# Performance work log

Hardware: AMD Instinct MI355X
Metric: run time of the kernel (lower is better)

## Reference

```python
import jax, jax.numpy as jnp
import numpy as np
from jax import lax

B, CIN, COUT, H, W = 8, 256, 256, 96, 96


def _conv_bn(x, w, g, b, act):
    # 3x3 conv, stride 1, SAME padding (NCHW / OIHW), then per-channel affine (folded BN)
    y = lax.conv_general_dilated(x, w, (1, 1), 'SAME',
                                 dimension_numbers=('NCHW', 'OIHW', 'NCHW'))
    y = y * g[None, :, None, None] + b[None, :, None, None]
    return jax.nn.relu(y) if act else y


def setup_inputs() -> dict:
    key = jax.random.key(0)
    ks = jax.random.split(key, 16)
    def wgt(k, cout, cin):
        return jax.random.normal(k, (cout, cin, 3, 3), jnp.float32) * (1.0 / np.sqrt(cin * 9))
    def gb(k, c):
        k1, k2 = jax.random.split(k)
        return (1.0 + 0.1 * jax.random.normal(k1, (c,), jnp.float32),
                0.1 * jax.random.normal(k2, (c,), jnp.float32))
    g_p1, b_p1 = gb(ks[1], COUT); g_p2, b_p2 = gb(ks[3], COUT)
    g_p, b_p = gb(ks[5], COUT); g_c1, b_c1 = gb(ks[7], COUT); g_c2, b_c2 = gb(ks[9], COUT)
    return {
        'x': jax.random.normal(ks[0], (B, CIN, H, W), jnp.float32),
        'w_p1': wgt(ks[10], COUT, CIN), 'g_p1': g_p1, 'b_p1': b_p1,
        'w_p2': wgt(ks[11], COUT, CIN), 'g_p2': g_p2, 'b_p2': b_p2,
        'w_p': wgt(ks[12], COUT, COUT), 'g_p': g_p, 'b_p': b_p,
        'w_c1': wgt(ks[13], COUT, CIN), 'g_c1': g_c1, 'b_c1': b_c1,
        'w_c2': wgt(ks[14], COUT, COUT), 'g_c2': g_c2, 'b_c2': b_c2,
    }


def reference(x, w_p1, g_p1, b_p1, w_p2, g_p2, b_p2, w_p, g_p, b_p,
              w_c1, g_c1, b_c1, w_c2, g_c2, b_c2):
    # branch 1: conv -> TopPool (cummax up, i.e. reverse along H) -> BottomPool (cummax down)
    p1 = _conv_bn(x, w_p1, g_p1, b_p1, act=True)
    pool1 = lax.cummax(p1, axis=2, reverse=True)   # TopPool
    pool1 = lax.cummax(pool1, axis=2)              # BottomPool
    # branch 2: conv -> LeftPool (reverse along W) -> RightPool
    p2 = _conv_bn(x, w_p2, g_p2, b_p2, act=True)
    pool2 = lax.cummax(p2, axis=3, reverse=True)   # LeftPool
    pool2 = lax.cummax(pool2, axis=3)              # RightPool
    p_conv = _conv_bn(pool1 + pool2, w_p, g_p, b_p, act=False)
    conv1 = _conv_bn(x, w_c1, g_c1, b_c1, act=False)
    relu = jax.nn.relu(p_conv + conv1)
    return _conv_bn(relu, w_c2, g_c2, b_c2, act=True)
```

## Files before the change

kernel.cpp:

```cpp
#include <hip/hip_runtime.h>


typedef _Float16 f16x8 __attribute__((ext_vector_type(8)));
typedef _Float16 f16x4v __attribute__((ext_vector_type(4)));
typedef float f32x4 __attribute__((ext_vector_type(4)));

#define HP 98
#define WP 98
#define KTOT 2304
#define WSET (256*KTOT)
#define XPAD_E ((size_t)8*HP*WP*256)
#define UVP_E  ((size_t)8*98*256)
#define UV2_E  ((size_t)3*8*96*256)
#define WUV_SET 196608

__device__ __forceinline__ int xcd_swz(int bid, int nwg)
{
  return (bid & 7) * (nwg >> 3) + (bid >> 3);
}

#define BUF_Q 24576
#define SMEM_Q 49152

struct CtxQ {
  unsigned goff[6];
  unsigned lds_stage;
  unsigned aoff;
  int wl, quad, wv;
  int b, h0, w0;
};

template<int SW>
__device__ __forceinline__ CtxQ make_ctxQ(int spatial, int ch)
{
  CtxQ c;
  c.b = spatial / 36;
  const int tt = spatial - c.b * 36;
  const int ht = tt / 6, wt = tt - ht * 6;
  c.h0 = ht * 16; c.w0 = wt * 16;
  const int tid = threadIdx.x, lane = tid & 63;
  c.wv = tid >> 6;
  c.quad = lane >> 4; c.wl = lane & 15;
  c.aoff = (unsigned)((ch * 8 + c.wv * 2) * 512 + c.wl * 32 + c.quad * 8);
  const unsigned base_hw = (unsigned)(c.b * HP + c.h0) * WP + c.w0;
#pragma unroll
  for (int t = 0; t < 6; ++t) {
    int s = (c.wv * 6 + t) * 16 + (lane >> 2);
    if (s > 323) s = 323;
    const int x = s / 18, y = s - x * 18;
    const int wh = SW ? y : x, ww = SW ? x : y;
    c.goff[t] = (base_hw + (unsigned)(wh * WP + ww)) * 256u + (lane & 3) * 8u;
  }
  c.lds_stage = (unsigned)(c.wv * 6) * 1024u + (unsigned)lane * 16u;
  return c;
}

__device__ __forceinline__ void stage_cbQ(const _Float16* __restrict__ src,
                                          char* sbuf, const CtxQ& c, int buf, int cb)
{
  char* l0 = sbuf + buf * BUF_Q + c.lds_stage;
#pragma unroll
  for (int t = 0; t < 6; ++t) {
    const _Float16* g = src + c.goff[t] + cb * 32;
    __builtin_amdgcn_global_load_lds(
        (const __attribute__((address_space(1))) void*)g,
        (__attribute__((address_space(3))) void*)(l0 + t * 1024), 16, 0, 0);
  }
}

template<int TR>
__device__ __forceinline__ void conv_accumQ(const _Float16* __restrict__ src,
                                            const _Float16* __restrict__ wkb,
                                            char* sbuf, const CtxQ& c, f32x4 acc[2][16])
{
  const _Float16* A0 = wkb + c.aoff;
  stage_cbQ(src, sbuf, c, 0, 0);
#pragma unroll 1
  for (int cb = 0; cb < 8; ++cb) {
    __syncthreads();
    if (cb < 7) stage_cbQ(src, sbuf, c, (cb + 1) & 1, cb + 1);
    const _Float16* B = (const _Float16*)(sbuf + (cb & 1) * BUF_Q);
    const _Float16* A = A0 + cb * (9 * 8192);
#pragma unroll
    for (int o = 0; o < 3; ++o) {
      f16x8 af[3][2];
#pragma unroll
      for (int p = 0; p < 3; ++p) {
        const int tap = (TR == 0) ? p * 3 + o : o * 3 + p;
#pragma unroll
        for (int i = 0; i < 2; ++i)
          af[p][i] = *(const f16x8*)(A + tap * 8192 + i * 512);
      }
#pragma unroll
      for (int jh = 0; jh < 2; ++jh) {
        f16x8 cache[10];
#pragma unroll
        for (int r = 0; r < 10; ++r)
          cache[r] = *(const f16x8*)(B + ((jh * 8 + r) * 18 + c.wl + o) * 32 + c.quad * 8);
#pragma unroll
        for (int p = 0; p < 3; ++p)
#pragma unroll
          for (int i = 0; i < 2; ++i)
#pragma unroll
            for (int j = 0; j < 8; ++j)
              acc[i][jh * 8 + j] = __builtin_amdgcn_mfma_f32_16x16x32_f16(
                  af[p][i], cache[j + p], acc[i][jh * 8 + j], 0, 0, 0);
      }
    }
  }
  __syncthreads();
}

#define BUF_W 7168
#define SMEM_W 14336

struct Ctx4 {
  unsigned goff[2];
  unsigned lds_stage;
  unsigned aoff;
  int nrow;
  int wl, quad, wv;
  int b, h0, w0;
};

__device__ __forceinline__ Ctx4 make_ctx4(int spatial)
{
  Ctx4 c;
  c.b = spatial / 144;
  const int tt = spatial - c.b * 144;
  const int ht = tt / 6,  wt = tt - ht * 6;  c.h0 = ht * 4;  c.w0 = wt * 16;
  const int tid = threadIdx.x, lane = tid & 63;
  c.wv = tid >> 6;
  c.quad = lane >> 4; c.wl = lane & 15;
  c.aoff = (unsigned)(c.wv * 4 * 512 + c.wl * 32 + c.quad * 8);
  const unsigned base_hw = (unsigned)(c.b * HP + c.h0) * WP + c.w0;
  const int r0 = c.wv * 2;
  c.nrow = (c.wv < 3) ? 2 : 1;
#pragma unroll
  for (int t = 0; t < 2; ++t) {
    int row = r0 + t; if (row > 6) row = 6;
    int pos = row * 16 + (lane >> 2);
    if (pos > 107) pos = 107;
    const int wh = pos / 18, ww = pos - wh * 18;
    c.goff[t] = (base_hw + (unsigned)(wh * WP + ww)) * 256u + (lane & 3) * 8u;
  }
  c.lds_stage = (unsigned)r0 * 1024u + (unsigned)lane * 16u;
  return c;
}

__device__ __forceinline__ void stage_cb4(const _Float16* __restrict__ src,
                                          char* sbuf, const Ctx4& c, int buf, int cb)
{
  char* l0 = sbuf + buf * BUF_W + c.lds_stage;
#pragma unroll
  for (int t = 0; t < 2; ++t) {
    if (t < c.nrow) {
      const _Float16* g = src + c.goff[t] + cb * 32;
      __builtin_amdgcn_global_load_lds(
          (const __attribute__((address_space(1))) void*)g,
          (__attribute__((address_space(3))) void*)(l0 + t * 1024), 16, 0, 0);
    }
  }
}

__device__ __forceinline__ void conv_accum4(const _Float16* __restrict__ src,
                                            const _Float16* __restrict__ wkb,
                                            char* sbuf, const Ctx4& c, f32x4 acc[4][4])
{
  const _Float16* A0 = wkb + c.aoff;
  stage_cb4(src, sbuf, c, 0, 0);
#pragma unroll 1
  for (int cb = 0; cb < 8; ++cb) {
    __syncthreads();
    if (cb < 7) stage_cb4(src, sbuf, c, (cb + 1) & 1, cb + 1);
    const _Float16* B = (const _Float16*)(sbuf + (cb & 1) * BUF_W);
    const _Float16* A = A0 + cb * (9 * 8192);
#pragma unroll
    for (int o = 0; o < 3; ++o) {
      f16x8 cache[6];
#pragma unroll
      for (int r = 0; r < 6; ++r)
        cache[r] = *(const f16x8*)(B + (r * 18 + c.wl + o) * 32 + c.quad * 8);
#pragma unroll
      for (int p = 0; p < 3; ++p) {
        const int tap = p * 3 + o;
        f16x8 af[4];
#pragma unroll
        for (int i = 0; i < 4; ++i)
          af[i] = *(const f16x8*)(A + tap * 8192 + i * 512);
#pragma unroll
        for (int i = 0; i < 4; ++i)
#pragma unroll
          for (int j = 0; j < 4; ++j)
            acc[i][j] = __builtin_amdgcn_mfma_f32_16x16x32_f16(af[i], cache[j + p], acc[i][j], 0, 0, 0);
      }
    }
  }
  __syncthreads();
}

__global__ __launch_bounds__(256, 2) void k_conv_p12(
    const _Float16* __restrict__ xpad, const _Float16* __restrict__ wk,
    const float* __restrict__ bias1, const float* __restrict__ bias2,
    float* __restrict__ u_pad, float* __restrict__ v_pad)
{
  __shared__ __align__(16) char smem[SMEM_Q];
  const int lin = xcd_swz(blockIdx.x, 1152);
  const int set = lin >= 576;
  const int rem = lin - set * 576;
  const int spatial = rem >> 1, ch = rem & 1;
  f32x4 acc[2][16];
#pragma unroll
  for (int i = 0; i < 2; ++i)
#pragma unroll
    for (int j = 0; j < 16; ++j) acc[i][j] = (f32x4){0.f, 0.f, 0.f, 0.f};
  if (set == 0) {
    CtxQ c = make_ctxQ<0>(spatial, ch);
    conv_accumQ<0>(xpad, wk, smem, c, acc);
#pragma unroll
    for (int i = 0; i < 2; ++i) {
      const int co = (ch * 8 + c.wv * 2 + i) * 16 + c.quad * 4;
      const float4 bs = *(const float4*)(bias1 + co);
      float m0 = 0.f, m1 = 0.f, m2 = 0.f, m3 = 0.f;
#pragma unroll
      for (int j = 0; j < 16; ++j) {
        m0 = fmaxf(m0, acc[i][j][0] + bs.x);
        m1 = fmaxf(m1, acc[i][j][1] + bs.y);
        m2 = fmaxf(m2, acc[i][j][2] + bs.z);
        m3 = fmaxf(m3, acc[i][j][3] + bs.w);
      }
      unsigned* tgt = (unsigned*)(u_pad + ((size_t)c.b * 98 + (c.w0 + c.wl + 1)) * 256 + co);
      atomicMax(tgt + 0, __float_as_uint(m0));
      atomicMax(tgt + 1, __float_as_uint(m1));
      atomicMax(tgt + 2, __float_as_uint(m2));
      atomicMax(tgt + 3, __float_as_uint(m3));
    }
  } else {
    CtxQ c = make_ctxQ<1>(spatial, ch);
    conv_accumQ<1>(xpad, wk + WSET, smem, c, acc);
#pragma unroll
    for (int i = 0; i < 2; ++i) {
      const int co = (ch * 8 + c.wv * 2 + i) * 16 + c.quad * 4;
      const float4 bs = *(const float4*)(bias2 + co);
      float m0 = 0.f, m1 = 0.f, m2 = 0.f, m3 = 0.f;
#pragma unroll
      for (int j = 0; j < 16; ++j) {
        m0 = fmaxf(m0, acc[i][j][0] + bs.x);
        m1 = fmaxf(m1, acc[i][j][1] + bs.y);
        m2 = fmaxf(m2, acc[i][j][2] + bs.z);
        m3 = fmaxf(m3, acc[i][j][3] + bs.w);
      }
      unsigned* tgt = (unsigned*)(v_pad + ((size_t)c.b * 98 + (c.h0 + c.wl + 1)) * 256 + co);
      atomicMax(tgt + 0, __float_as_uint(m0));
      atomicMax(tgt + 1, __float_as_uint(m1));
      atomicMax(tgt + 2, __float_as_uint(m2));
      atomicMax(tgt + 3, __float_as_uint(m3));
    }
  }
}

__global__ __launch_bounds__(256, 2) void k_uv1d(
    const float* __restrict__ u_pad, const float* __restrict__ v_pad,
    const _Float16* __restrict__ wuv, float* __restrict__ u2, float* __restrict__ v2)
{
  const int id = blockIdx.x;
  const int b = id & 7, cs = (id >> 3) % 3, t = id / 24;
  const float* src = t ? v_pad : u_pad;
  float* dst = t ? v2 : u2;
  const _Float16* A0 = wuv + (size_t)(t * 3 + cs) * WUV_SET;
  const int lane = threadIdx.x & 63, wv = threadIdx.x >> 6;
  const int quad = lane >> 4, l16 = lane & 15;

  f32x4 acc[4][6];
#pragma unroll
  for (int i = 0; i < 4; ++i)
#pragma unroll
    for (int j = 0; j < 6; ++j) acc[i][j] = (f32x4){0.f, 0.f, 0.f, 0.f};

#pragma unroll 1
  for (int kb = 0; kb < 24; ++kb) {
    const int dw = kb >> 3, cb = kb & 7;
    f16x8 bf[6];
#pragma unroll
    for (int j = 0; j < 6; ++j) {
      const int pos = j * 16 + l16;
      const float* p = src + ((size_t)b * 98 + (pos + dw)) * 256 + cb * 32 + quad * 8;
      const float4 x0 = *(const float4*)p;
      const float4 x1 = *(const float4*)(p + 4);
      f16x8 v;
      v[0] = (_Float16)x0.x; v[1] = (_Float16)x0.y; v[2] = (_Float16)x0.z; v[3] = (_Float16)x0.w;
      v[4] = (_Float16)x1.x; v[5] = (_Float16)x1.y; v[6] = (_Float16)x1.z; v[7] = (_Float16)x1.w;
      bf[j] = v;
    }
    f16x8 af[4];
#pragma unroll
    for (int i = 0; i < 4; ++i)
      af[i] = *(const f16x8*)(A0 + (size_t)(kb * 16 + wv * 4 + i) * 512 + l16 * 32 + quad * 8);
#pragma unroll
    for (int i = 0; i < 4; ++i)
#pragma unroll
      for (int j = 0; j < 6; ++j)
        acc[i][j] = __builtin_amdgcn_mfma_f32_16x16x32_f16(af[i], bf[j], acc[i][j], 0, 0, 0);
  }
#pragma unroll
  for (int i = 0; i < 4; ++i)
#pragma unroll
    for (int j = 0; j < 6; ++j) {
      const int pos = j * 16 + l16;
      const int co = wv * 64 + i * 16 + quad * 4;
      *(f32x4*)(dst + ((size_t)(cs * 8 + b) * 96 + pos) * 256 + co) = acc[i][j];
    }
}

__global__ __launch_bounds__(256, 3) void k_conv_c1f(
    const _Float16* __restrict__ xpad, const _Float16* __restrict__ wkc1,
    const float* __restrict__ bias_p, const float* __restrict__ bias_c1,
    const float* __restrict__ u2, const float* __restrict__ v2,
    _Float16* __restrict__ rpad)
{
  __shared__ __align__(16) char smem[SMEM_W];
  const int lin = xcd_swz(blockIdx.x, 1152);
  Ctx4 c = make_ctx4(lin);
  f32x4 acc[4][4];
#pragma unroll
  for (int i = 0; i < 4; ++i)
#pragma unroll
    for (int j = 0; j < 4; ++j) acc[i][j] = (f32x4){0.f, 0.f, 0.f, 0.f};
  conv_accum4(xpad, wkc1, smem, c, acc);

  const int w = c.w0 + c.wl;
  const int wcase = (w == 0) ? 0 : ((w == 95) ? 2 : 1);
#pragma unroll
  for (int i = 0; i < 4; ++i) {
    const int co = c.wv * 64 + i * 16 + c.quad * 4;
    float4 bs = *(const float4*)(bias_p + co);
    const float4 b2 = *(const float4*)(bias_c1 + co);
    bs.x += b2.x; bs.y += b2.y; bs.z += b2.z; bs.w += b2.w;
#pragma unroll
    for (int j = 0; j < 4; ++j) {
      const int h = c.h0 + j;
      const int hcase = (h == 0) ? 0 : ((h == 95) ? 2 : 1);
      const float4 uq = *(const float4*)(u2 + ((size_t)(hcase * 8 + c.b) * 96 + w) * 256 + co);
      const float4 vq = *(const float4*)(v2 + ((size_t)(wcase * 8 + c.b) * 96 + h) * 256 + co);
      f16x4v pk;
      pk[0] = (_Float16)fmaxf(acc[i][j][0] + bs.x + uq.x + vq.x, 0.f);
      pk[1] = (_Float16)fmaxf(acc[i][j][1] + bs.y + uq.y + vq.y, 0.f);
      pk[2] = (_Float16)fmaxf(acc[i][j][2] + bs.z + uq.z + vq.z, 0.f);
      pk[3] = (_Float16)fmaxf(acc[i][j][3] + bs.w + uq.w + vq.w, 0.f);
      *(f16x4v*)(rpad + ((size_t)(c.b * HP + h + 1) * WP + w + 1) * 256 + co) = pk;
    }
  }
}

__global__ __launch_bounds__(256, 3) void k_conv_c2(
    const _Float16* __restrict__ rpad, const _Float16* __restrict__ wkc2,
    const float* __restrict__ bias, float* __restrict__ dout)
{
  __shared__ __align__(16) char smem[SMEM_W];
  const int lin = xcd_swz(blockIdx.x, 1152);
  Ctx4 c = make_ctx4(lin);
  f32x4 acc[4][4];
#pragma unroll
  for (int i = 0; i < 4; ++i)
#pragma unroll
    for (int j = 0; j < 4; ++j) acc[i][j] = (f32x4){0.f, 0.f, 0.f, 0.f};
  conv_accum4(rpad, wkc2, smem, c, acc);

  const int w = c.w0 + c.wl;
#pragma unroll
  for (int j = 0; j < 4; ++j) {
    const int h = c.h0 + j;
    float* op = dout + (size_t)c.b * 2359296 + h * 96 + w;
#pragma unroll
    for (int i = 0; i < 4; ++i) {
      const int co = c.wv * 64 + i * 16 + c.quad * 4;
      const float4 bs = *(const float4*)(bias + co);
      op[(size_t)(co + 0) * 9216] = fmaxf(acc[i][j][0] + bs.x, 0.f);
      op[(size_t)(co + 1) * 9216] = fmaxf(acc[i][j][1] + bs.y, 0.f);
      op[(size_t)(co + 2) * 9216] = fmaxf(acc[i][j][2] + bs.z, 0.f);
      op[(size_t)(co + 3) * 9216] = fmaxf(acc[i][j][3] + bs.w, 0.f);
    }
  }
}

__global__ void k_border(_Float16* __restrict__ xpad, _Float16* __restrict__ rpad)
{
  const int idx = blockIdx.x, b = blockIdx.y;
  _Float16* buf = blockIdx.z ? rpad : xpad;
  int h, w;
  if (idx < 98)       { h = 0;  w = idx; }
  else if (idx < 196) { h = 97; w = idx - 98; }
  else { const int r = idx - 196; h = 1 + (r >> 1); w = (r & 1) ? 97 : 0; }
  buf[((size_t)(b * HP + h) * WP + w) * 256 + threadIdx.x] = (_Float16)0.f;
}

__global__ void k_pack_x(const float* __restrict__ x, _Float16* __restrict__ xpad)
{
  __shared__ float tile[32][33];
  const int bh = blockIdx.x;
  const int b = bh / 96, h = bh - b * 96;
  const int c0 = blockIdx.y * 32, w0 = blockIdx.z * 32;
  const int tx = threadIdx.x & 31, ty = threadIdx.x >> 5;
#pragma unroll
  for (int i = 0; i < 4; ++i) {
    int cI = c0 + ty + i * 8;
    tile[ty + i * 8][tx] = x[(((size_t)b * 256 + cI) * 96 + h) * 96 + w0 + tx];
  }
  __syncthreads();
#pragma unroll
  for (int i = 0; i < 4; ++i) {
    int w = w0 + ty + i * 8;
    xpad[((size_t)(b * HP + h + 1) * WP + (w + 1)) * 256 + c0 + tx] =
        (_Float16)tile[tx][ty + i * 8];
  }
}

__global__ void k_repack_w(const float* w0, const float* g0, const float* w1, const float* g1,
                           const float* w2, const float* g2, const float* w3, const float* g3,
                           const float* w4, const float* g4, _Float16* __restrict__ wk)
{
  const int set = blockIdx.y;
  const float* w; const float* g;
  switch (set) {
    case 0: w = w0; g = g0; break;
    case 1: w = w1; g = g1; break;
    case 2: w = w2; g = g2; break;
    case 3: w = w3; g = g3; break;
    default: w = w4; g = g4; break;
  }
  const int t = blockIdx.x * 256 + threadIdx.x;
  const int co = t >> 8, ci = t & 255;
  const int cb = ci >> 5, kk = ci & 31, cog = co >> 4, m = co & 15;
  const float gv = g[co];
  const float* src = w + ((size_t)co * 256 + ci) * 9;
  _Float16* dst = wk + (size_t)set * WSET + cog * 512 + m * 32 + kk;
#pragma unroll
  for (int tap = 0; tap < 9; ++tap)
    dst[(cb * 9 + tap) * 8192] = (_Float16)(src[tap] * gv);
}

__global__ void k_repack_uvw(const float* __restrict__ wp, const float* __restrict__ gp,
                             _Float16* __restrict__ wuv)
{
  const int tcs = blockIdx.y;
  const int tt = tcs / 3, cs = tcs - tt * 3;
  const int idx = blockIdx.x * 256 + threadIdx.x;
  const int co = idx >> 8, ci = idx & 255;
  const float gv = gp[co];
  const float* src = wp + ((size_t)co * 256 + ci) * 9;
  const int lo = (cs == 0) ? 1 : 0, hi = (cs == 2) ? 1 : 2;
  _Float16* base = wuv + (size_t)tcs * WUV_SET;
#pragma unroll
  for (int d = 0; d < 3; ++d) {
    float s = 0.f;
    for (int e = lo; e <= hi; ++e)
      s += (tt == 0) ? src[e * 3 + d] : src[d * 3 + e];
    const int k = d * 256 + ci;
    const int kb = k >> 5, kk = k & 31;
    base[(size_t)(kb * 16 + (co >> 4)) * 512 + (co & 15) * 32 + kk] = (_Float16)(s * gv);
  }
}

extern "C" void kernel_launch(void* const* d_in, const int* in_sizes, int n_in,
                              void* d_out, int out_size, void* d_ws, size_t ws_size,
                              hipStream_t stream)
{
  const float* x    = (const float*)d_in[0];
  const float* w_p1 = (const float*)d_in[1];
  const float* g_p1 = (const float*)d_in[2];
  const float* b_p1 = (const float*)d_in[3];
  const float* w_p2 = (const float*)d_in[4];
  const float* g_p2 = (const float*)d_in[5];
  const float* b_p2 = (const float*)d_in[6];
  const float* w_p  = (const float*)d_in[7];
  const float* g_p  = (const float*)d_in[8];
  const float* b_p  = (const float*)d_in[9];
  const float* w_c1 = (const float*)d_in[10];
  const float* g_c1 = (const float*)d_in[11];
  const float* b_c1 = (const float*)d_in[12];
  const float* w_c2 = (const float*)d_in[13];
  const float* g_c2 = (const float*)d_in[14];
  const float* b_c2 = (const float*)d_in[15];

  char* ws = (char*)d_ws;
  size_t off = 0;
  _Float16* x_pad = (_Float16*)(ws + off); off += XPAD_E * 2;
  _Float16* r_pad = (_Float16*)(ws + off); off += XPAD_E * 2;
  _Float16* wks   = (_Float16*)(ws + off); off += (size_t)5 * WSET * 2;
  _Float16* wuv   = (_Float16*)(ws + off); off += (size_t)6 * WUV_SET * 2;
  float*    u_pad = (float*)(ws + off);    off += UVP_E * 4;
  float*    v_pad = (float*)(ws + off);    off += UVP_E * 4;
  float*    u2    = (float*)(ws + off);    off += UV2_E * 4;
  float*    v2    = (float*)(ws + off);    off += UV2_E * 4;
  (void)ws_size; (void)in_sizes; (void)n_in; (void)out_size;

  hipMemsetAsync(u_pad, 0, UVP_E * 4, stream);
  hipMemsetAsync(v_pad, 0, UVP_E * 4, stream);

  k_border    <<<dim3(388, 8, 2), 256, 0, stream>>>(x_pad, r_pad);
  k_pack_x    <<<dim3(768, 8, 3), 256, 0, stream>>>(x, x_pad);
  k_repack_w  <<<dim3(256, 5),    256, 0, stream>>>(w_p1, g_p1, w_p2, g_p2, w_p, g_p,
                                                    w_c1, g_c1, w_c2, g_c2, wks);
  k_repack_uvw<<<dim3(256, 6),    256, 0, stream>>>(w_p, g_p, wuv);
  k_conv_p12  <<<1152, 256, 0, stream>>>(x_pad, wks, b_p1, b_p2, u_pad, v_pad);
  k_uv1d      <<<48,   256, 0, stream>>>(u_pad, v_pad, wuv, u2, v2);
  k_conv_c1f  <<<1152, 256, 0, stream>>>(x_pad, wks + (size_t)3 * WSET, b_p, b_c1,
                                         u2, v2, r_pad);
  k_conv_c2   <<<1152, 256, 0, stream>>>(r_pad, wks + (size_t)4 * WSET, b_c2,
                                         (float*)d_out);
}
```

Measured before the change: 560.6 us.

## Switch c1 and c2 convolutions to the larger Q tile used by p12

The c1-fused and c2 conv kernels move from the small 4x16-pixel, 256-channel tile path (Ctx4/conv_accum4) to the larger CtxQ/conv_accumQ tiling already used by the p12 kernel. Each block now covers a bigger spatial region with half the output channels, which raises input and weight reuse per LDS stage. The grid shrinks from 1152 to 576 blocks and occupancy drops from 3 to 2 blocks per CU. The trade is fewer, heavier blocks with more registers and LDS, which may leave the GPU less filled or cause wave-quantization imbalance.

```diff
diff --git a/kernel.cpp b/kernel.cpp
--- a/kernel.cpp
+++ b/kernel.cpp
@@ -111,93 +111,9 @@
   __syncthreads();
 }
 
-#define BUF_W 7168
-#define SMEM_W 14336
-
-struct Ctx4 {
-  unsigned goff[2];
-  unsigned lds_stage;
-  unsigned aoff;
-  int nrow;
-  int wl, quad, wv;
-  int b, h0, w0;
-};
-
-__device__ __forceinline__ Ctx4 make_ctx4(int spatial)
-{
-  Ctx4 c;
-  c.b = spatial / 144;
-  const int tt = spatial - c.b * 144;
-  const int ht = tt / 6,  wt = tt - ht * 6;  c.h0 = ht * 4;  c.w0 = wt * 16;
-  const int tid = threadIdx.x, lane = tid & 63;
-  c.wv = tid >> 6;
-  c.quad = lane >> 4; c.wl = lane & 15;
-  c.aoff = (unsigned)(c.wv * 4 * 512 + c.wl * 32 + c.quad * 8);
-  const unsigned base_hw = (unsigned)(c.b * HP + c.h0) * WP + c.w0;
-  const int r0 = c.wv * 2;
-  c.nrow = (c.wv < 3) ? 2 : 1;
-#pragma unroll
-  for (int t = 0; t < 2; ++t) {
-    int row = r0 + t; if (row > 6) row = 6;
-    int pos = row * 16 + (lane >> 2);
-    if (pos > 107) pos = 107;
-    const int wh = pos / 18, ww = pos - wh * 18;
-    c.goff[t] = (base_hw + (unsigned)(wh * WP + ww)) * 256u + (lane & 3) * 8u;
-  }
-  c.lds_stage = (unsigned)r0 * 1024u + (unsigned)lane * 16u;
-  return c;
-}
-
-__device__ __forceinline__ void stage_cb4(const _Float16* __restrict__ src,
-                                          char* sbuf, const Ctx4& c, int buf, int cb)
-{
-  char* l0 = sbuf + buf * BUF_W + c.lds_stage;
-#pragma unroll
-  for (int t = 0; t < 2; ++t) {
-    if (t < c.nrow) {
-      const _Float16* g = src + c.goff[t] + cb * 32;
-      __builtin_amdgcn_global_load_lds(
-          (const __attribute__((address_space(1))) void*)g,
-          (__attribute__((address_space(3))) void*)(l0 + t * 1024), 16, 0, 0);
-    }
-  }
-}
-
-__device__ __forceinline__ void conv_accum4(const _Float16* __restrict__ src,
-                                            const _Float16* __restrict__ wkb,
-                                            char* sbuf, const Ctx4& c, f32x4 acc[4][4])
-{
-  const _Float16* A0 = wkb + c.aoff;
-  stage_cb4(src, sbuf, c, 0, 0);
-#pragma unroll 1
-  for (int cb = 0; cb < 8; ++cb) {
-    __syncthreads();
-    if (cb < 7) stage_cb4(src, sbuf, c, (cb + 1) & 1, cb + 1);
-    const _Float16* B = (const _Float16*)(sbuf + (cb & 1) * BUF_W);
-    const _Float16* A = A0 + cb * (9 * 8192);
-#pragma unroll
-    for (int o = 0; o < 3; ++o) {
-      f16x8 cache[6];
-#pragma unroll
-      for (int r = 0; r < 6; ++r)
-        cache[r] = *(const f16x8*)(B + (r * 18 + c.wl + o) * 32 + c.quad * 8);
-#pragma unroll
-      for (int p = 0; p < 3; ++p) {
-        const int tap = p * 3 + o;
-        f16x8 af[4];
-#pragma unroll
-        for (int i = 0; i < 4; ++i)
-          af[i] = *(const f16x8*)(A + tap * 8192 + i * 512);
-#pragma unroll
-        for (int i = 0; i < 4; ++i)
-#pragma unroll
-          for (int j = 0; j < 4; ++j)
-            acc[i][j] = __builtin_amdgcn_mfma_f32_16x16x32_f16(af[i], cache[j + p], acc[i][j], 0, 0, 0);
-      }
-    }
-  }
-  __syncthreads();
-}
+#define ZERO_ACCQ(acc) \
+  _Pragma("unroll") for (int i = 0; i < 2; ++i) \
+  _Pragma("unroll") for (int j = 0; j < 16; ++j) acc[i][j] = (f32x4){0.f,0.f,0.f,0.f};
 
 __global__ __launch_bounds__(256, 2) void k_conv_p12(
     const _Float16* __restrict__ xpad, const _Float16* __restrict__ wk,
@@ -210,10 +126,7 @@
   const int rem = lin - set * 576;
   const int spatial = rem >> 1, ch = rem & 1;
   f32x4 acc[2][16];
-#pragma unroll
-  for (int i = 0; i < 2; ++i)
-#pragma unroll
-    for (int j = 0; j < 16; ++j) acc[i][j] = (f32x4){0.f, 0.f, 0.f, 0.f};
+  ZERO_ACCQ(acc)
   if (set == 0) {
     CtxQ c = make_ctxQ<0>(spatial, ch);
     conv_accumQ<0>(xpad, wk, smem, c, acc);
@@ -312,32 +225,30 @@
     }
 }
 
-__global__ __launch_bounds__(256, 3) void k_conv_c1f(
+__global__ __launch_bounds__(256, 2) void k_conv_c1f(
     const _Float16* __restrict__ xpad, const _Float16* __restrict__ wkc1,
     const float* __restrict__ bias_p, const float* __restrict__ bias_c1,
     const float* __restrict__ u2, const float* __restrict__ v2,
     _Float16* __restrict__ rpad)
 {
-  __shared__ __align__(16) char smem[SMEM_W];
-  const int lin = xcd_swz(blockIdx.x, 1152);
-  Ctx4 c = make_ctx4(lin);
-  f32x4 acc[4][4];
-#pragma unroll
-  for (int i = 0; i < 4; ++i)
-#pragma unroll
-    for (int j = 0; j < 4; ++j) acc[i][j] = (f32x4){0.f, 0.f, 0.f, 0.f};
-  conv_accum4(xpad, wkc1, smem, c, acc);
+  __shared__ __align__(16) char smem[SMEM_Q];
+  const int lin = xcd_swz(blockIdx.x, 576);
+  const int spatial = lin >> 1, ch = lin & 1;
+  CtxQ c = make_ctxQ<0>(spatial, ch);
+  f32x4 acc[2][16];
+  ZERO_ACCQ(acc)
+  conv_accumQ<0>(xpad, wkc1, smem, c, acc);
 
   const int w = c.w0 + c.wl;
   const int wcase = (w == 0) ? 0 : ((w == 95) ? 2 : 1);
 #pragma unroll
-  for (int i = 0; i < 4; ++i) {
-    const int co = c.wv * 64 + i * 16 + c.quad * 4;
+  for (int i = 0; i < 2; ++i) {
+    const int co = (ch * 8 + c.wv * 2 + i) * 16 + c.quad * 4;
     float4 bs = *(const float4*)(bias_p + co);
     const float4 b2 = *(const float4*)(bias_c1 + co);
     bs.x += b2.x; bs.y += b2.y; bs.z += b2.z; bs.w += b2.w;
 #pragma unroll
-    for (int j = 0; j < 4; ++j) {
+    for (int j = 0; j < 16; ++j) {
       const int h = c.h0 + j;
       const int hcase = (h == 0) ? 0 : ((h == 95) ? 2 : 1);
       const float4 uq = *(const float4*)(u2 + ((size_t)(hcase * 8 + c.b) * 96 + w) * 256 + co);
@@ -352,28 +263,26 @@
   }
 }
 
-__global__ __launch_bounds__(256, 3) void k_conv_c2(
+__global__ __launch_bounds__(256, 2) void k_conv_c2(
     const _Float16* __restrict__ rpad, const _Float16* __restrict__ wkc2,
     const float* __restrict__ bias, float* __restrict__ dout)
 {
-  __shared__ __align__(16) char smem[SMEM_W];
-  const int lin = xcd_swz(blockIdx.x, 1152);
-  Ctx4 c = make_ctx4(lin);
-  f32x4 acc[4][4];
-#pragma unroll
-  for (int i = 0; i < 4; ++i)
-#pragma unroll
-    for (int j = 0; j < 4; ++j) acc[i][j] = (f32x4){0.f, 0.f, 0.f, 0.f};
-  conv_accum4(rpad, wkc2, smem, c, acc);
+  __shared__ __align__(16) char smem[SMEM_Q];
+  const int lin = xcd_swz(blockIdx.x, 576);
+  const int spatial = lin >> 1, ch = lin & 1;
+  CtxQ c = make_ctxQ<0>(spatial, ch);
+  f32x4 acc[2][16];
+  ZERO_ACCQ(acc)
+  conv_accumQ<0>(rpad, wkc2, smem, c, acc);
 
   const int w = c.w0 + c.wl;
 #pragma unroll
-  for (int j = 0; j < 4; ++j) {
+  for (int j = 0; j < 16; ++j) {
     const int h = c.h0 + j;
     float* op = dout + (size_t)c.b * 2359296 + h * 96 + w;
 #pragma unroll
-    for (int i = 0; i < 4; ++i) {
-      const int co = c.wv * 64 + i * 16 + c.quad * 4;
+    for (int i = 0; i < 2; ++i) {
+      const int co = (ch * 8 + c.wv * 2 + i) * 16 + c.quad * 4;
       const float4 bs = *(const float4*)(bias + co);
       op[(size_t)(co + 0) * 9216] = fmaxf(acc[i][j][0] + bs.x, 0.f);
       op[(size_t)(co + 1) * 9216] = fmaxf(acc[i][j][1] + bs.y, 0.f);
@@ -504,8 +413,8 @@
   k_repack_uvw<<<dim3(256, 6),    256, 0, stream>>>(w_p, g_p, wuv);
   k_conv_p12  <<<1152, 256, 0, stream>>>(x_pad, wks, b_p1, b_p2, u_pad, v_pad);
   k_uv1d      <<<48,   256, 0, stream>>>(u_pad, v_pad, wuv, u2, v2);
-  k_conv_c1f  <<<1152, 256, 0, stream>>>(x_pad, wks + (size_t)3 * WSET, b_p, b_c1,
+  k_conv_c1f  <<<576,  256, 0, stream>>>(x_pad, wks + (size_t)3 * WSET, b_p, b_c1,
                                          u2, v2, r_pad);
-  k_conv_c2   <<<1152, 256, 0, stream>>>(r_pad, wks + (size_t)4 * WSET, b_c2,
+  k_conv_c2   <<<576,  256, 0, stream>>>(r_pad, wks + (size_t)4 * WSET, b_c2,
                                          (float*)d_out);
 }
```

Measured after the change: 555.7 us. About the same (-0.9%).
